# Kernel optimization log

Hardware: AMD Instinct MI355X
Metric: run time of the kernel (lower is better)

## Reference

```python
import jax, jax.numpy as jnp
import numpy as np

B, S, D = 2, 2048, 2048
H = 16
Q_LORA, KV_LORA = 1536, 512
D_NOPE, D_ROPE, D_V = 128, 64, 128
D_QK = D_NOPE + D_ROPE  # 192
EPS = 1e-6


def rmsnorm(x, w):
    return x * jax.lax.rsqrt(jnp.mean(x * x, axis=-1, keepdims=True) + EPS) * w


def apply_rope(x, freqs_cis):
    # x: (B, S, h, D_ROPE); freqs_cis: (S, D_ROPE//2, 2) = (cos, sin)
    # DeepSeek pairs consecutive elements (2i, 2i+1) as complex re/im.
    b, s, h, d = x.shape
    xp = x.reshape(b, s, h, d // 2, 2)
    re, im = xp[..., 0], xp[..., 1]
    cos = freqs_cis[None, :, None, :, 0]
    sin = freqs_cis[None, :, None, :, 1]
    out_re = re * cos - im * sin
    out_im = re * sin + im * cos
    return jnp.stack([out_re, out_im], axis=-1).reshape(b, s, h, d)


def setup_inputs() -> dict:
    key = jax.random.key(0)
    ks = jax.random.split(key, 8)
    sd = 0.02
    x = jax.random.normal(ks[0], (B, S, D), dtype=jnp.float32)
    # RoPE table over the rope head dim
    inv_freq = 1.0 / (10000.0 ** (np.arange(0, D_ROPE, 2, dtype=np.float32) / D_ROPE))
    t = np.arange(S, dtype=np.float32)
    f = np.outer(t, inv_freq)  # (S, 32)
    freqs_cis = jnp.asarray(np.stack([np.cos(f), np.sin(f)], axis=-1), dtype=jnp.float32)
    return {
        "x": x,
        "start_pos": 0,
        "freqs_cis": freqs_cis,
        "wq_a": jax.random.normal(ks[1], (Q_LORA, D), dtype=jnp.float32) * sd,
        "q_norm_w": jnp.ones((Q_LORA,), dtype=jnp.float32),
        "wq_b": jax.random.normal(ks[2], (H * D_QK, Q_LORA), dtype=jnp.float32) * sd,
        "wkv_a": jax.random.normal(ks[3], (KV_LORA + D_ROPE, D), dtype=jnp.float32) * sd,
        "kv_norm_w": jnp.ones((KV_LORA,), dtype=jnp.float32),
        "wkv_b": jax.random.normal(ks[4], (H * (D_NOPE + D_V), KV_LORA), dtype=jnp.float32) * sd,
        "wo": jax.random.normal(ks[5], (D, H * D_V), dtype=jnp.float32) * sd,
    }


def reference(x, start_pos, freqs_cis, wq_a, q_norm_w, wq_b, wkv_a, kv_norm_w, wkv_b, wo):
    bsz, seqlen, _ = x.shape
    softmax_scale = D_QK ** (-0.5)

    # --- queries: low-rank down-proj, RMSNorm, up-proj ---
    q = rmsnorm(x @ wq_a.T, q_norm_w) @ wq_b.T          # (B,S,H*D_QK)
    q = q.reshape(bsz, seqlen, H, D_QK)
    q_nope, q_pe = q[..., :D_NOPE], q[..., D_NOPE:]
    q_pe = apply_rope(q_pe, freqs_cis)
    q = jnp.concatenate([q_nope, q_pe], axis=-1)         # (B,S,H,192)

    # --- keys/values: compressed latent + shared rope key ---
    kv = x @ wkv_a.T                                     # (B,S,KV_LORA+D_ROPE)
    kv_c, k_pe = kv[..., :KV_LORA], kv[..., KV_LORA:]
    k_pe = apply_rope(k_pe[:, :, None, :], freqs_cis)    # (B,S,1,64)
    kvb = rmsnorm(kv_c, kv_norm_w) @ wkv_b.T             # (B,S,H*(D_NOPE+D_V))
    kvb = kvb.reshape(bsz, seqlen, H, D_NOPE + D_V)
    k_nope, v = kvb[..., :D_NOPE], kvb[..., D_NOPE:]
    k = jnp.concatenate([k_nope, jnp.broadcast_to(k_pe, (bsz, seqlen, H, D_ROPE))], axis=-1)

    # --- causal attention (FA2 with attention_mask=None) ---
    scores = jnp.einsum("bqhd,bkhd->bhqk", q, k) * softmax_scale
    causal = jnp.tril(jnp.ones((seqlen, seqlen), dtype=bool))
    scores = jnp.where(causal[None, None], scores, jnp.finfo(scores.dtype).min)
    attn = jax.nn.softmax(scores, axis=-1)
    out = jnp.einsum("bhqk,bkhd->bqhd", attn, v)         # (B,S,H,D_V)
    # (v padding to qk_head_dim then slicing [..., :D_V] is a no-op)
    return out.reshape(bsz, seqlen, H * D_V) @ wo.T
```

## Files before the change

### kernel.cpp

```cpp
#include <hip/hip_runtime.h>
#include <math.h>

typedef short short8 __attribute__((ext_vector_type(8)));
typedef short short4v __attribute__((ext_vector_type(4)));
typedef float float4v __attribute__((ext_vector_type(4)));
#define AS1 __attribute__((address_space(1)))
#define AS3 __attribute__((address_space(3)))

__device__ __forceinline__ float b2f(ushort u) {
    unsigned v = ((unsigned)u) << 16; float f; __builtin_memcpy(&f, &v, 4); return f;
}
__device__ __forceinline__ ushort f2b(float f) {
    unsigned v; __builtin_memcpy(&v, &f, 4);
    unsigned r = (v + 0x7fffu + ((v >> 16) & 1u)) >> 16;
    return (ushort)r;
}

__device__ __forceinline__ float4v pv_mfma(short4v a, short4v b, float4v c) {
#if __has_builtin(__builtin_amdgcn_mfma_f32_16x16x16_bf16)
    return __builtin_amdgcn_mfma_f32_16x16x16_bf16(a, b, c, 0, 0, 0);
#elif __has_builtin(__builtin_amdgcn_mfma_f32_16x16x16bf16_1k)
    return __builtin_amdgcn_mfma_f32_16x16x16bf16_1k(a, b, c, 0, 0, 0);
#else
    short8 a8 = {a[0], a[1], a[2], a[3], 0, 0, 0, 0};
    short8 b8 = {b[0], b[1], b[2], b[3], 0, 0, 0, 0};
    return __builtin_amdgcn_mfma_f32_16x16x32_bf16(a8, b8, c, 0, 0, 0);
#endif
}

__global__ void cvt_pad(const float* __restrict__ src, ushort* __restrict__ dst,
                        int src_rows, int cols, int total4) {
    int i = blockIdx.x * 256 + threadIdx.x;
    if (i >= total4) return;
    size_t e = (size_t)i * 4;
    int r = (int)(e / (size_t)cols);
    ushort4 o;
    if (r < src_rows) {
        float4 v = *(const float4*)(src + e);
        o.x = f2b(v.x); o.y = f2b(v.y); o.z = f2b(v.z); o.w = f2b(v.w);
    } else {
        o.x = 0; o.y = 0; o.z = 0; o.w = 0;
    }
    *(ushort4*)(dst + e) = o;
}

__global__ __launch_bounds__(256)
void gemm_bt(const ushort* __restrict__ A, const ushort* __restrict__ B,
             void* __restrict__ Cv, int K, int lda, int ldb, int ldc, int f32out) {
    __shared__ ushort sA[128 * 32];
    __shared__ ushort sB[128 * 32];
    const int tid = threadIdx.x;
    const int wave = tid >> 6, lane = tid & 63;
    const int bm = blockIdx.y * 128, bn = blockIdx.x * 128;
    const int wm = (wave >> 1) * 64, wn = (wave & 1) * 64;
    float4v acc[4][4] = {};

    const int srow = wave * 32 + (lane >> 2);
    const int skc = (lane & 3) * 8;
    const ushort* Ag = A + (size_t)(bm + srow) * lda + skc;
    const ushort* Bg = B + (size_t)(bn + srow) * ldb + skc;
    ushort* sAw = sA + (wave * 32) * 32;
    ushort* sBw = sB + (wave * 32) * 32;

    for (int k0 = 0; k0 < K; k0 += 32) {
        __builtin_amdgcn_global_load_lds((const AS1 void*)(Ag + k0), (AS3 void*)sAw, 16, 0, 0);
        __builtin_amdgcn_global_load_lds((const AS1 void*)(Ag + (size_t)16 * lda + k0),
                                         (AS3 void*)(sAw + 16 * 32), 16, 0, 0);
        __builtin_amdgcn_global_load_lds((const AS1 void*)(Bg + k0), (AS3 void*)sBw, 16, 0, 0);
        __builtin_amdgcn_global_load_lds((const AS1 void*)(Bg + (size_t)16 * ldb + k0),
                                         (AS3 void*)(sBw + 16 * 32), 16, 0, 0);
        __syncthreads();
        short8 af[4], bfr[4];
#pragma unroll
        for (int i = 0; i < 4; ++i) {
            af[i]  = *(const short8*)(sA + (wm + i * 16 + (lane & 15)) * 32 + (lane >> 4) * 8);
            bfr[i] = *(const short8*)(sB + (wn + i * 16 + (lane & 15)) * 32 + (lane >> 4) * 8);
        }
#pragma unroll
        for (int i = 0; i < 4; ++i)
#pragma unroll
            for (int j = 0; j < 4; ++j)
                acc[i][j] = __builtin_amdgcn_mfma_f32_16x16x32_bf16(af[i], bfr[j], acc[i][j], 0, 0, 0);
        __syncthreads();
    }
#pragma unroll
    for (int i = 0; i < 4; ++i) {
        int row0 = bm + wm + i * 16 + (lane >> 4) * 4;
#pragma unroll
        for (int j = 0; j < 4; ++j) {
            int col = bn + wn + j * 16 + (lane & 15);
            if (f32out) {
                float* C = (float*)Cv;
#pragma unroll
                for (int r = 0; r < 4; ++r)
                    C[(size_t)(row0 + r) * ldc + col] = acc[i][j][r];
            } else {
                ushort* C = (ushort*)Cv;
#pragma unroll
                for (int r = 0; r < 4; ++r)
                    C[(size_t)(row0 + r) * ldc + col] = f2b(acc[i][j][r]);
            }
        }
    }
}

__global__ void rmsnorm_inplace(ushort* __restrict__ d, const float* __restrict__ w,
                                int cols, int ld) {
    int row = blockIdx.x, tid = threadIdx.x;
    ushort* p = d + (size_t)row * ld;
    float ss = 0.f;
    for (int i = tid; i < cols; i += 256) { float v = b2f(p[i]); ss += v * v; }
#pragma unroll
    for (int off = 32; off >= 1; off >>= 1) ss += __shfl_xor(ss, off);
    __shared__ float red[4];
    if ((tid & 63) == 0) red[tid >> 6] = ss;
    __syncthreads();
    float tot = red[0] + red[1] + red[2] + red[3];
    float rs = rsqrtf(tot / (float)cols + 1e-6f);
    for (int i = tid; i < cols; i += 256) p[i] = f2b(b2f(p[i]) * rs * w[i]);
}

__global__ void kvnorm_rope(const ushort* __restrict__ kvraw, const float* __restrict__ w,
                            const float* __restrict__ freqs, ushort* __restrict__ kvc,
                            ushort* __restrict__ kpe, int ld) {
    int row = blockIdx.x, tid = threadIdx.x;
    int s = row & 2047;
    const ushort* p = kvraw + (size_t)row * ld;
    float v0 = b2f(p[tid]), v1 = b2f(p[tid + 256]);
    float ss = v0 * v0 + v1 * v1;
#pragma unroll
    for (int off = 32; off >= 1; off >>= 1) ss += __shfl_xor(ss, off);
    __shared__ float red[4];
    if ((tid & 63) == 0) red[tid >> 6] = ss;
    __syncthreads();
    float tot = red[0] + red[1] + red[2] + red[3];
    float rs = rsqrtf(tot / 512.f + 1e-6f);
    kvc[(size_t)row * 512 + tid] = f2b(v0 * rs * w[tid]);
    kvc[(size_t)row * 512 + tid + 256] = f2b(v1 * rs * w[tid + 256]);
    if (tid < 32) {
        float re = b2f(p[512 + 2 * tid]), im = b2f(p[512 + 2 * tid + 1]);
        float cs = freqs[(s * 32 + tid) * 2], sn = freqs[(s * 32 + tid) * 2 + 1];
        kpe[(size_t)row * 64 + 2 * tid] = f2b(re * cs - im * sn);
        kpe[(size_t)row * 64 + 2 * tid + 1] = f2b(re * sn + im * cs);
    }
}

__global__ void qrope(ushort* __restrict__ q, const float* __restrict__ freqs) {
    int idx = blockIdx.x * 256 + threadIdx.x;
    int i = idx & 31;
    int h = (idx >> 5) & 15;
    int srow = idx >> 9;
    int s = srow & 2047;
    ushort* p = q + ((size_t)srow * 16 + h) * 192 + 128 + 2 * i;
    float re = b2f(p[0]), im = b2f(p[1]);
    float cs = freqs[(s * 32 + i) * 2], sn = freqs[(s * 32 + i) * 2 + 1];
    p[0] = f2b(re * cs - im * sn);
    p[1] = f2b(re * sn + im * cs);
}

__global__ void k_repack(const ushort* __restrict__ kvb, const ushort* __restrict__ kpe,
                         ushort* __restrict__ Kfull) {
    int tid = threadIdx.x;
    int row = blockIdx.x * 8 + (tid >> 5);
    int c = tid & 31;
    int bh = row >> 11, s = row & 2047;
    int b = bh >> 4, h = bh & 15;
    size_t sg = (size_t)b * 2048 + s;
    short8 v = {0, 0, 0, 0, 0, 0, 0, 0};
    if (c < 16)      v = *(const short8*)(kvb + sg * 4096 + h * 256 + c * 8);
    else if (c < 24) v = *(const short8*)(kpe + sg * 64 + (c - 16) * 8);
    if (c < 25) *(short8*)(Kfull + (size_t)row * 200 + c * 8) = v;
}

__global__ __launch_bounds__(256)
void v_repack(const ushort* __restrict__ kvb, ushort* __restrict__ Vt) {
    __shared__ ushort sT[64][136];
    int tid = threadIdx.x;
    int kt = blockIdx.x, bh = blockIdx.y;
    int b = bh >> 4, h = bh & 15;
#pragma unroll
    for (int k = 0; k < 4; ++k) {
        int id = k * 256 + tid;
        int r = id >> 4, c8 = id & 15;
        size_t sg = (size_t)b * 2048 + kt * 64 + r;
        *(short8*)(&sT[r][c8 * 8]) = *(const short8*)(kvb + sg * 4096 + h * 256 + 128 + c8 * 8);
    }
    __syncthreads();
    int d = tid >> 1, half = tid & 1;
    ushort tmp[32];
#pragma unroll
    for (int i = 0; i < 32; ++i) tmp[i] = sT[half * 32 + i][d];
    ushort* dst = Vt + (((size_t)bh * 32 + kt) * 128 + d) * 72 + half * 32;
#pragma unroll
    for (int i = 0; i < 4; ++i) *(short8*)(dst + i * 8) = *(const short8*)(tmp + i * 8);
}

__global__ __launch_bounds__(256)
void mla_attn3(const ushort* __restrict__ q, const ushort* __restrict__ Kfull,
               const ushort* __restrict__ Vt, ushort* __restrict__ out, float scale) {
    __shared__ ushort sK[64 * 200];
    __shared__ ushort sV[128 * 72];
    const int tid = threadIdx.x, wave = tid >> 6, lane = tid & 63;
    const int lq = lane & 15, quad = lane >> 4;
    const int qt = 31 - blockIdx.x;
    const int bh = blockIdx.y;
    const int b = bh >> 4, h = bh & 15;
    const ushort* Kb = Kfull + (size_t)bh * 2048 * 200;
    const ushort* Vb = Vt + (size_t)bh * 32 * 128 * 72;

    const int q_abs = qt * 64 + wave * 16 + lq;
    const ushort* qp = q + ((size_t)(b * 2048 + q_abs) * 16 + h) * 192 + quad * 8;
    short8 qf[6];
#pragma unroll
    for (int c = 0; c < 6; ++c) qf[c] = *(const short8*)(qp + c * 32);

    float4v oacc[8] = {};
    float m_i = -INFINITY, l_i = 0.f;

    for (int kt = 0; kt <= qt; ++kt) {
        const ushort* Ksrc = Kb + (size_t)kt * 64 * 200;
        const ushort* Vsrc = Vb + (size_t)kt * 128 * 72;
#pragma unroll
        for (int i = 0; i < 7; ++i) {
            int s0 = i * 256 + wave * 64;
            if (s0 < 1600)
                __builtin_amdgcn_global_load_lds((const AS1 void*)(Ksrc + (size_t)(s0 + lane) * 8),
                                                 (AS3 void*)(sK + s0 * 8), 16, 0, 0);
        }
#pragma unroll
        for (int i = 0; i < 5; ++i) {
            int s0 = i * 256 + wave * 64;
            if (s0 < 1152)
                __builtin_amdgcn_global_load_lds((const AS1 void*)(Vsrc + (size_t)(s0 + lane) * 8),
                                                 (AS3 void*)(sV + s0 * 8), 16, 0, 0);
        }
        __syncthreads();
        float4v sc[4];
#pragma unroll
        for (int ct = 0; ct < 4; ++ct) {
            float4v a = {0.f, 0.f, 0.f, 0.f};
#pragma unroll
            for (int c = 0; c < 6; ++c) {
                short8 kf = *(const short8*)(sK + (ct * 16 + lq) * 200 + c * 32 + quad * 8);
                a = __builtin_amdgcn_mfma_f32_16x16x32_bf16(kf, qf[c], a, 0, 0, 0);
            }
            sc[ct] = a;
        }
        float mx = m_i;
#pragma unroll
        for (int ct = 0; ct < 4; ++ct)
#pragma unroll
            for (int r = 0; r < 4; ++r) {
                float v = sc[ct][r] * scale;
                int kv = kt * 64 + ct * 16 + quad * 4 + r;
                if (kv > q_abs) v = -INFINITY;
                sc[ct][r] = v;
                mx = fmaxf(mx, v);
            }
        mx = fmaxf(mx, __shfl_xor(mx, 16));
        mx = fmaxf(mx, __shfl_xor(mx, 32));
        float alpha = __expf(m_i - mx);
        m_i = mx;
        float ps = 0.f;
        short4v pf[4];
#pragma unroll
        for (int ct = 0; ct < 4; ++ct)
#pragma unroll
            for (int r = 0; r < 4; ++r) {
                float pv = __expf(sc[ct][r] - mx);
                ps += pv;
                pf[ct][r] = (short)f2b(pv);
            }
        ps += __shfl_xor(ps, 16);
        ps += __shfl_xor(ps, 32);
        l_i = l_i * alpha + ps;
#pragma unroll
        for (int dt = 0; dt < 8; ++dt)
#pragma unroll
            for (int r = 0; r < 4; ++r) oacc[dt][r] *= alpha;
#pragma unroll
        for (int dt = 0; dt < 8; ++dt)
#pragma unroll
            for (int ct = 0; ct < 4; ++ct) {
                short4v vf = *(const short4v*)(sV + (dt * 16 + lq) * 72 + ct * 16 + quad * 4);
                oacc[dt] = pv_mfma(vf, pf[ct], oacc[dt]);
            }
        __syncthreads();
    }
    float inv = 1.f / l_i;
#pragma unroll
    for (int dt = 0; dt < 8; ++dt) {
        ushort4 o;
        o.x = f2b(oacc[dt][0] * inv);
        o.y = f2b(oacc[dt][1] * inv);
        o.z = f2b(oacc[dt][2] * inv);
        o.w = f2b(oacc[dt][3] * inv);
        *(ushort4*)(out + ((size_t)(b * 2048 + q_abs) * 16 + h) * 128 + dt * 16 + quad * 4) = o;
    }
}

extern "C" void kernel_launch(void* const* d_in, const int* in_sizes, int n_in,
                              void* d_out, int out_size, void* d_ws, size_t ws_size,
                              hipStream_t stream) {
    const float* x     = (const float*)d_in[0];
    const float* freqs = (const float*)d_in[2];
    const float* wq_a  = (const float*)d_in[3];
    const float* qnw   = (const float*)d_in[4];
    const float* wq_b  = (const float*)d_in[5];
    const float* wkv_a = (const float*)d_in[6];
    const float* kvnw  = (const float*)d_in[7];
    const float* wkv_b = (const float*)d_in[8];
    const float* wo    = (const float*)d_in[9];

    char* ws = (char*)d_ws;
    size_t off = 0;
    auto alloc = [&](size_t n) { char* p = ws + off; off += (n + 255) & ~(size_t)255; return p; };
    ushort* xb    = (ushort*)alloc(4096ull * 2048 * 2);
    ushort* wqkva = (ushort*)alloc(2176ull * 2048 * 2);
    ushort* wqbb  = (ushort*)alloc(3072ull * 1536 * 2);
    ushort* wkvbb = (ushort*)alloc(4096ull * 512 * 2);
    ushort* wob   = (ushort*)alloc(2048ull * 2048 * 2);
    ushort* qakv  = (ushort*)alloc(4096ull * 2176 * 2);
    ushort* kvc   = (ushort*)alloc(4096ull * 512 * 2);
    ushort* kpe   = (ushort*)alloc(4096ull * 64 * 2);
    ushort* qfull = (ushort*)alloc(4096ull * 3072 * 2);
    ushort* kvbuf = (ushort*)alloc(4096ull * 4096 * 2);
    ushort* attno = (ushort*)alloc(4096ull * 2048 * 2);
    if (off > ws_size) return;
    ushort* Kfull = (ushort*)xb;
    ushort* Vt = (ushort*)qakv;

    auto cvt = [&](const float* s, ushort* dd, int sr, int cols, size_t dtot) {
        int t4 = (int)(dtot / 4);
        cvt_pad<<<(t4 + 255) / 256, 256, 0, stream>>>(s, dd, sr, cols, t4);
    };
    cvt(x, xb, 4096, 2048, 4096ull * 2048);
    cvt(wq_a, wqkva, 1536, 2048, 1536ull * 2048);
    cvt(wkv_a, wqkva + 1536ull * 2048, 576, 2048, 640ull * 2048);
    cvt(wq_b, wqbb, 3072, 1536, 3072ull * 1536);
    cvt(wkv_b, wkvbb, 4096, 512, 4096ull * 512);
    cvt(wo, wob, 2048, 2048, 2048ull * 2048);

    gemm_bt<<<dim3(17, 32), 256, 0, stream>>>(xb, wqkva, qakv, 2048, 2048, 2048, 2176, 0);
    rmsnorm_inplace<<<4096, 256, 0, stream>>>(qakv, qnw, 1536, 2176);
    kvnorm_rope<<<4096, 256, 0, stream>>>(qakv + 1536, kvnw, freqs, kvc, kpe, 2176);
    gemm_bt<<<dim3(24, 32), 256, 0, stream>>>(qakv, wqbb, qfull, 1536, 2176, 1536, 3072, 0);
    qrope<<<8192, 256, 0, stream>>>(qfull, freqs);
    gemm_bt<<<dim3(32, 32), 256, 0, stream>>>(kvc, wkvbb, kvbuf, 512, 512, 512, 4096, 0);
    k_repack<<<8192, 256, 0, stream>>>(kvbuf, kpe, Kfull);
    v_repack<<<dim3(32, 32), 256, 0, stream>>>(kvbuf, Vt);
    const float scale = 1.0f / sqrtf(192.0f);
    mla_attn3<<<dim3(32, 32), 256, 0, stream>>>(qfull, Kfull, Vt, attno, scale);
    gemm_bt<<<dim3(16, 32), 256, 0, stream>>>(attno, wob, (float*)d_out, 2048, 2048, 2048, 2048, 1);
}
```

Baseline: 561.3 us.

## Process 128 query rows per block with two groups per wave, staging P through LDS

The attention kernel now gives each wave two 16-row query groups, so one block covers 128 queries and every K/V tile loaded into LDS is reused by twice as many rows. The QK product is transposed so scores are row-major per lane. P is written to shared memory and read back as short8 fragments, which lets the PV product use the wider 16x16x32 MFMA instead of the 16x16x16 variant. The causal mask is applied only on diagonal tiles. In exchange there are more registers per thread, an extra barrier per tile, larger LDS use, and half as many blocks, which gives coarser causal load balance.

```diff
diff --git a/kernel.cpp b/kernel.cpp
--- a/kernel.cpp
+++ b/kernel.cpp
@@ -2,7 +2,6 @@
 #include <math.h>
 
 typedef short short8 __attribute__((ext_vector_type(8)));
-typedef short short4v __attribute__((ext_vector_type(4)));
 typedef float float4v __attribute__((ext_vector_type(4)));
 #define AS1 __attribute__((address_space(1)))
 #define AS3 __attribute__((address_space(3)))
@@ -14,18 +13,6 @@
     unsigned v; __builtin_memcpy(&v, &f, 4);
     unsigned r = (v + 0x7fffu + ((v >> 16) & 1u)) >> 16;
     return (ushort)r;
-}
-
-__device__ __forceinline__ float4v pv_mfma(short4v a, short4v b, float4v c) {
-#if __has_builtin(__builtin_amdgcn_mfma_f32_16x16x16_bf16)
-    return __builtin_amdgcn_mfma_f32_16x16x16_bf16(a, b, c, 0, 0, 0);
-#elif __has_builtin(__builtin_amdgcn_mfma_f32_16x16x16bf16_1k)
-    return __builtin_amdgcn_mfma_f32_16x16x16bf16_1k(a, b, c, 0, 0, 0);
-#else
-    short8 a8 = {a[0], a[1], a[2], a[3], 0, 0, 0, 0};
-    short8 b8 = {b[0], b[1], b[2], b[3], 0, 0, 0, 0};
-    return __builtin_amdgcn_mfma_f32_16x16x32_bf16(a8, b8, c, 0, 0, 0);
-#endif
 }
 
 __global__ void cvt_pad(const float* __restrict__ src, ushort* __restrict__ dst,
@@ -195,29 +182,38 @@
     for (int i = 0; i < 4; ++i) *(short8*)(dst + i * 8) = *(const short8*)(tmp + i * 8);
 }
 
-__global__ __launch_bounds__(256)
-void mla_attn3(const ushort* __restrict__ q, const ushort* __restrict__ Kfull,
+__global__ __launch_bounds__(256, 2)
+void mla_attn4(const ushort* __restrict__ q, const ushort* __restrict__ Kfull,
                const ushort* __restrict__ Vt, ushort* __restrict__ out, float scale) {
     __shared__ ushort sK[64 * 200];
     __shared__ ushort sV[128 * 72];
+    __shared__ ushort sP[4 * 32 * 72];
     const int tid = threadIdx.x, wave = tid >> 6, lane = tid & 63;
     const int lq = lane & 15, quad = lane >> 4;
-    const int qt = 31 - blockIdx.x;
+    const int qt = 15 - blockIdx.x;
     const int bh = blockIdx.y;
     const int b = bh >> 4, h = bh & 15;
     const ushort* Kb = Kfull + (size_t)bh * 2048 * 200;
     const ushort* Vb = Vt + (size_t)bh * 32 * 128 * 72;
 
-    const int q_abs = qt * 64 + wave * 16 + lq;
-    const ushort* qp = q + ((size_t)(b * 2048 + q_abs) * 16 + h) * 192 + quad * 8;
-    short8 qf[6];
-#pragma unroll
-    for (int c = 0; c < 6; ++c) qf[c] = *(const short8*)(qp + c * 32);
-
-    float4v oacc[8] = {};
-    float m_i = -INFINITY, l_i = 0.f;
-
-    for (int kt = 0; kt <= qt; ++kt) {
+    short8 qf[2][6];
+#pragma unroll
+    for (int g = 0; g < 2; ++g) {
+        int qrow = qt * 128 + (wave * 2 + g) * 16 + lq;
+        const ushort* qp = q + ((size_t)(b * 2048 + qrow) * 16 + h) * 192 + quad * 8;
+#pragma unroll
+        for (int c = 0; c < 6; ++c) qf[g][c] = *(const short8*)(qp + c * 32);
+    }
+
+    float4v oacc[2][8] = {};
+    float m_i[2][4], l_i[2][4];
+#pragma unroll
+    for (int g = 0; g < 2; ++g)
+#pragma unroll
+        for (int r = 0; r < 4; ++r) { m_i[g][r] = -INFINITY; l_i[g][r] = 0.f; }
+
+    const int nkt = 2 * qt + 2;
+    for (int kt = 0; kt < nkt; ++kt) {
         const ushort* Ksrc = Kb + (size_t)kt * 64 * 200;
         const ushort* Vsrc = Vb + (size_t)kt * 128 * 72;
 #pragma unroll
@@ -235,67 +231,90 @@
                                                  (AS3 void*)(sV + s0 * 8), 16, 0, 0);
         }
         __syncthreads();
-        float4v sc[4];
+        float4v sc[2][4];
 #pragma unroll
         for (int ct = 0; ct < 4; ++ct) {
-            float4v a = {0.f, 0.f, 0.f, 0.f};
+            float4v a0 = {0.f, 0.f, 0.f, 0.f}, a1 = {0.f, 0.f, 0.f, 0.f};
 #pragma unroll
             for (int c = 0; c < 6; ++c) {
                 short8 kf = *(const short8*)(sK + (ct * 16 + lq) * 200 + c * 32 + quad * 8);
-                a = __builtin_amdgcn_mfma_f32_16x16x32_bf16(kf, qf[c], a, 0, 0, 0);
-            }
-            sc[ct] = a;
-        }
-        float mx = m_i;
-#pragma unroll
-        for (int ct = 0; ct < 4; ++ct)
+                a0 = __builtin_amdgcn_mfma_f32_16x16x32_bf16(qf[0][c], kf, a0, 0, 0, 0);
+                a1 = __builtin_amdgcn_mfma_f32_16x16x32_bf16(qf[1][c], kf, a1, 0, 0, 0);
+            }
+            sc[0][ct] = a0;
+            sc[1][ct] = a1;
+        }
+        const int edge = ((kt >> 1) == qt);
+#pragma unroll
+        for (int g = 0; g < 2; ++g) {
+            const int myrow0 = qt * 128 + (wave * 2 + g) * 16 + quad * 4;
+            float mnew[4];
+#pragma unroll
+            for (int r = 0; r < 4; ++r) mnew[r] = m_i[g][r];
+#pragma unroll
+            for (int ct = 0; ct < 4; ++ct)
+#pragma unroll
+                for (int r = 0; r < 4; ++r) {
+                    float v = sc[g][ct][r] * scale;
+                    if (edge && (kt * 64 + ct * 16 + lq) > (myrow0 + r)) v = -INFINITY;
+                    sc[g][ct][r] = v;
+                    mnew[r] = fmaxf(mnew[r], v);
+                }
+#pragma unroll
+            for (int off = 8; off >= 1; off >>= 1)
+#pragma unroll
+                for (int r = 0; r < 4; ++r) mnew[r] = fmaxf(mnew[r], __shfl_xor(mnew[r], off));
+            float alpha[4], psum[4];
 #pragma unroll
             for (int r = 0; r < 4; ++r) {
-                float v = sc[ct][r] * scale;
-                int kv = kt * 64 + ct * 16 + quad * 4 + r;
-                if (kv > q_abs) v = -INFINITY;
-                sc[ct][r] = v;
-                mx = fmaxf(mx, v);
-            }
-        mx = fmaxf(mx, __shfl_xor(mx, 16));
-        mx = fmaxf(mx, __shfl_xor(mx, 32));
-        float alpha = __expf(m_i - mx);
-        m_i = mx;
-        float ps = 0.f;
-        short4v pf[4];
-#pragma unroll
-        for (int ct = 0; ct < 4; ++ct)
+                alpha[r] = __expf(m_i[g][r] - mnew[r]);
+                m_i[g][r] = mnew[r];
+                psum[r] = 0.f;
+            }
+#pragma unroll
+            for (int ct = 0; ct < 4; ++ct)
+#pragma unroll
+                for (int r = 0; r < 4; ++r) {
+                    float pv = __expf(sc[g][ct][r] - mnew[r]);
+                    psum[r] += pv;
+                    sP[(wave * 32 + g * 16 + quad * 4 + r) * 72 + ct * 16 + lq] = f2b(pv);
+                }
+#pragma unroll
+            for (int off = 8; off >= 1; off >>= 1)
+#pragma unroll
+                for (int r = 0; r < 4; ++r) psum[r] += __shfl_xor(psum[r], off);
+#pragma unroll
+            for (int r = 0; r < 4; ++r) l_i[g][r] = l_i[g][r] * alpha[r] + psum[r];
+#pragma unroll
+            for (int dt = 0; dt < 8; ++dt)
+#pragma unroll
+                for (int r = 0; r < 4; ++r) oacc[g][dt][r] *= alpha[r];
+        }
+        __syncthreads();
+#pragma unroll
+        for (int kc = 0; kc < 2; ++kc) {
+            short8 pf0 = *(const short8*)(sP + (wave * 32 + lq) * 72 + kc * 32 + quad * 8);
+            short8 pf1 = *(const short8*)(sP + (wave * 32 + 16 + lq) * 72 + kc * 32 + quad * 8);
+#pragma unroll
+            for (int dt = 0; dt < 8; ++dt) {
+                short8 vf = *(const short8*)(sV + (dt * 16 + lq) * 72 + kc * 32 + quad * 8);
+                oacc[0][dt] = __builtin_amdgcn_mfma_f32_16x16x32_bf16(pf0, vf, oacc[0][dt], 0, 0, 0);
+                oacc[1][dt] = __builtin_amdgcn_mfma_f32_16x16x32_bf16(pf1, vf, oacc[1][dt], 0, 0, 0);
+            }
+        }
+        __syncthreads();
+    }
+#pragma unroll
+    for (int g = 0; g < 2; ++g) {
+        const int myrow0 = qt * 128 + (wave * 2 + g) * 16 + quad * 4;
+#pragma unroll
+        for (int dt = 0; dt < 8; ++dt) {
 #pragma unroll
             for (int r = 0; r < 4; ++r) {
-                float pv = __expf(sc[ct][r] - mx);
-                ps += pv;
-                pf[ct][r] = (short)f2b(pv);
-            }
-        ps += __shfl_xor(ps, 16);
-        ps += __shfl_xor(ps, 32);
-        l_i = l_i * alpha + ps;
-#pragma unroll
-        for (int dt = 0; dt < 8; ++dt)
-#pragma unroll
-            for (int r = 0; r < 4; ++r) oacc[dt][r] *= alpha;
-#pragma unroll
-        for (int dt = 0; dt < 8; ++dt)
-#pragma unroll
-            for (int ct = 0; ct < 4; ++ct) {
-                short4v vf = *(const short4v*)(sV + (dt * 16 + lq) * 72 + ct * 16 + quad * 4);
-                oacc[dt] = pv_mfma(vf, pf[ct], oacc[dt]);
-            }
-        __syncthreads();
-    }
-    float inv = 1.f / l_i;
-#pragma unroll
-    for (int dt = 0; dt < 8; ++dt) {
-        ushort4 o;
-        o.x = f2b(oacc[dt][0] * inv);
-        o.y = f2b(oacc[dt][1] * inv);
-        o.z = f2b(oacc[dt][2] * inv);
-        o.w = f2b(oacc[dt][3] * inv);
-        *(ushort4*)(out + ((size_t)(b * 2048 + q_abs) * 16 + h) * 128 + dt * 16 + quad * 4) = o;
+                out[((size_t)(b * 2048 + myrow0 + r) * 16 + h) * 128 + dt * 16 + lq] =
+                    f2b(oacc[g][dt][r] / l_i[g][r]);
+            }
+        }
     }
 }
 
@@ -350,6 +369,6 @@
     k_repack<<<8192, 256, 0, stream>>>(kvbuf, kpe, Kfull);
     v_repack<<<dim3(32, 32), 256, 0, stream>>>(kvbuf, Vt);
     const float scale = 1.0f / sqrtf(192.0f);
-    mla_attn3<<<dim3(32, 32), 256, 0, stream>>>(qfull, Kfull, Vt, attno, scale);
+    mla_attn4<<<dim3(16, 32), 256, 0, stream>>>(qfull, Kfull, Vt, attno, scale);
     gemm_bt<<<dim3(16, 32), 256, 0, stream>>>(attno, wob, (float*)d_out, 2048, 2048, 2048, 2048, 1);
 }
```

Result: slower. 584.3 us (+4.1%).
